# Kernel tuning notes

Hardware: AMD Instinct MI355X
Metric: run time of the kernel (lower is better)

The kernel has to match this reference:

```python
import jax, jax.numpy as jnp
import numpy as np

NUM_GRAPHS = 128
NUM_LAYERS = 3
BN_EPS = 1e-5


def setup_inputs() -> dict:
    key = jax.random.key(0)
    ks = jax.random.split(key, 8)
    N, E, D, C = 100000, 1250000, 64, 10
    x = jax.random.normal(ks[0], (N, D), dtype=jnp.float32)
    edge_index = jax.random.randint(ks[1], (2, E), 0, N, dtype=jnp.int64)
    batch = jnp.sort(jax.random.randint(ks[2], (N,), 0, NUM_GRAPHS, dtype=jnp.int64))
    W_rel = jax.random.normal(ks[3], (NUM_LAYERS, D, D), dtype=jnp.float32) * (1.0 / np.sqrt(D))
    b_rel = jax.random.normal(ks[4], (NUM_LAYERS, D), dtype=jnp.float32) * 0.01
    W_root = jax.random.normal(ks[5], (NUM_LAYERS, D, D), dtype=jnp.float32) * (1.0 / np.sqrt(D))
    gamma = jnp.ones((NUM_LAYERS, D), dtype=jnp.float32)
    beta = jnp.zeros((NUM_LAYERS, D), dtype=jnp.float32)
    W_cls = jax.random.normal(ks[6], (D, C), dtype=jnp.float32) * (1.0 / np.sqrt(D))
    b_cls = jnp.zeros((C,), dtype=jnp.float32)
    return {"x": x, "edge_index": edge_index, "batch": batch,
            "W_rel": W_rel, "b_rel": b_rel, "W_root": W_root,
            "gamma": gamma, "beta": beta, "W_cls": W_cls, "b_cls": b_cls}


def reference(x, edge_index, batch, W_rel, b_rel, W_root, gamma, beta, W_cls, b_cls):
    N = x.shape[0]
    src, dst = edge_index[0], edge_index[1]
    for l in range(NUM_LAYERS):
        # GraphConv: lin_rel(sum-aggregated neighbor feats) + lin_root(x)
        msg = jax.ops.segment_sum(x[src], dst, num_segments=N)  # [N, D]
        h = msg @ W_rel[l] + b_rel[l] + x @ W_root[l]
        # BatchNorm1d over nodes (batch statistics, training-mode math)
        mean = jnp.mean(h, axis=0)
        var = jnp.var(h, axis=0)
        h = (h - mean) * jax.lax.rsqrt(var + BN_EPS) * gamma[l] + beta[l]
        x = jax.nn.relu(h)  # dropout is identity at inference
    # global_mean_pool: segment mean over graph ids
    counts = jax.ops.segment_sum(jnp.ones((N,), dtype=x.dtype), batch, num_segments=NUM_GRAPHS)
    pooled = jax.ops.segment_sum(x, batch, num_segments=NUM_GRAPHS)
    pooled = pooled / jnp.maximum(counts, 1.0)[:, None]  # [G, D]
    return pooled @ W_cls + b_cls
```

## Files before the change

kernel.cpp:

```cpp
#include <hip/hip_runtime.h>

#define D 64
#define NGRAPH 128
#define NCLS 10
#define BN_EPS 1e-5f
#define BUCK_SZ 512
#define EPB 8192

typedef __attribute__((ext_vector_type(8))) __bf16 bf16x8;
typedef __attribute__((ext_vector_type(4))) float floatx4;

union BF8 { bf16x8 v; ushort u[8]; };

__device__ __forceinline__ unsigned f2bf_rne(float f) {
  unsigned u = __float_as_uint(f);
  return (u + 0x7FFFu + ((u >> 16) & 1u)) >> 16;
}
__device__ __forceinline__ unsigned pack2bf(float a, float b) {
  return f2bf_rne(a) | (f2bf_rne(b) << 16);
}
__device__ __forceinline__ float4 bf4_to_f4(uint2 u) {
  float4 r;
  r.x = __uint_as_float(u.x << 16);
  r.y = __uint_as_float(u.x & 0xFFFF0000u);
  r.z = __uint_as_float(u.y << 16);
  r.w = __uint_as_float(u.y & 0xFFFF0000u);
  return r;
}

__device__ __forceinline__ void split8(float4 a, float4 b,
                                       bf16x8* hi, bf16x8* lo) {
  float f[8] = {a.x, a.y, a.z, a.w, b.x, b.y, b.z, b.w};
  BF8 H, L;
#pragma unroll
  for (int t = 0; t < 8; t++) {
    unsigned u = __float_as_uint(f[t]);
    H.u[t] = (ushort)(u >> 16);
    float hf = __uint_as_float(u & 0xFFFF0000u);
    float lf = f[t] - hf;
    L.u[t] = (ushort)(__float_as_uint(lf) >> 16);
  }
  *hi = H.v;
  *lo = L.v;
}

__global__ __launch_bounds__(256) void bucket_scatter_kernel(
    const int* __restrict__ ei, int* __restrict__ gcnt, int* __restrict__ pk,
    int E, int capB, int nbuck) {
  __shared__ int hist[256];
  __shared__ int base[256];
  int t = threadIdx.x;
  int e0 = blockIdx.x * EPB;
  int e1 = min(e0 + EPB, E);
  hist[t] = 0;
  __syncthreads();
  for (int e = e0 + t; e < e1; e += 256)
    atomicAdd(&hist[ei[E + e] >> 9], 1);
  __syncthreads();
  int h = hist[t];
  if (t < nbuck && h > 0) base[t] = atomicAdd(&gcnt[t], h);
  hist[t] = 0;
  __syncthreads();
  for (int e = e0 + t; e < e1; e += 256) {
    int s = ei[e];
    int d = ei[E + e];
    int b = d >> 9;
    int pos = base[b] + atomicAdd(&hist[b], 1);
    if (pos < capB) pk[(size_t)b * capB + pos] = (s << 9) | (d & (BUCK_SZ - 1));
  }
}

__global__ void bucket_scan_kernel(const int* __restrict__ gcnt,
                                   int* __restrict__ bstart,
                                   int* __restrict__ row_start,
                                   int nbuck, int N, int capB) {
  __shared__ int s[256];
  int t = threadIdx.x;
  int v = (t < nbuck) ? min(gcnt[t], capB) : 0;
  s[t] = v;
  __syncthreads();
  for (int off = 1; off < 256; off <<= 1) {
    int add = (t >= off) ? s[t - off] : 0;
    __syncthreads();
    s[t] += add;
    __syncthreads();
  }
  if (t < nbuck) bstart[t] = s[t] - v;
  if (t == 0) {
    bstart[nbuck] = s[255];
    row_start[N] = s[255];
  }
}

__global__ __launch_bounds__(256) void bucket_place_kernel(
    const int* __restrict__ pk, const int* __restrict__ gcnt,
    const int* __restrict__ bstart, int* __restrict__ row_start,
    int* __restrict__ csr_src, int N, int capB) {
  __shared__ int hist[BUCK_SZ];
  __shared__ int scn[256];
  __shared__ int cur[BUCK_SZ];
  int b = blockIdx.x;
  int t = threadIdx.x;
  hist[t] = 0;
  hist[t + 256] = 0;
  int cnt = min(gcnt[b], capB);
  const int* seg = pk + (size_t)b * capB;
  __syncthreads();
  for (int e = t; e < cnt; e += 256)
    atomicAdd(&hist[seg[e] & (BUCK_SZ - 1)], 1);
  __syncthreads();
  scn[t] = hist[2 * t] + hist[2 * t + 1];
  __syncthreads();
  for (int off = 1; off < 256; off <<= 1) {
    int add = (t >= off) ? scn[t - off] : 0;
    __syncthreads();
    scn[t] += add;
    __syncthreads();
  }
  int base = bstart[b];
  int ex = (t == 0) ? 0 : scn[t - 1];
  int c0 = base + ex;
  int c1 = c0 + hist[2 * t];
  cur[2 * t] = c0;
  cur[2 * t + 1] = c1;
  int dst0 = b * BUCK_SZ + 2 * t;
  if (dst0 < N) row_start[dst0] = c0;
  if (dst0 + 1 < N) row_start[dst0 + 1] = c1;
  __syncthreads();
  for (int e = t; e < cnt; e += 256) {
    int p = seg[e];
    int slot = atomicAdd(&cur[p & (BUCK_SZ - 1)], 1);
    csr_src[slot] = p >> 9;
  }
}

__global__ __launch_bounds__(256) void wsplit_kernel(
    const float* __restrict__ Wrel, const float* __restrict__ Wroot,
    ushort* __restrict__ wfrag) {
  int l = blockIdx.x;
  const float* Wr = Wrel + l * 4096;
  const float* Wo = Wroot + l * 4096;
  ushort* base = wfrag + l * 16384;
  for (int slot = threadIdx.x; slot < 1024; slot += 256) {
    int kt = slot >> 8, nt = (slot >> 6) & 3, lane = slot & 63;
    int quad = lane >> 4, c = lane & 15;
    ushort* ph = base + (((kt * 4 + nt) * 2 + 0) * 64 + lane) * 8;
    ushort* pl = base + (((kt * 4 + nt) * 2 + 1) * 64 + lane) * 8;
#pragma unroll
    for (int j = 0; j < 8; j++) {
      int k = kt * 32 + quad * 8 + j;
      int n = nt * 16 + c;
      float w = (k < 64) ? Wr[k * 64 + n] : Wo[(k - 64) * 64 + n];
      unsigned u = __float_as_uint(w);
      ph[j] = (ushort)(u >> 16);
      float lf = w - __uint_as_float(u & 0xFFFF0000u);
      pl[j] = (ushort)(__float_as_uint(lf) >> 16);
    }
  }
}

__global__ __launch_bounds__(256) void xprep_kernel(
    const float* __restrict__ x, ushort* __restrict__ xbf, int n) {
  int base = (blockIdx.x * 256 + threadIdx.x) * 8;
  if (base >= n) return;
  float4 a = *(const float4*)(x + base);
  float4 b = *(const float4*)(x + base + 4);
  uint4 o;
  o.x = pack2bf(a.x, a.y);
  o.y = pack2bf(a.z, a.w);
  o.z = pack2bf(b.x, b.y);
  o.w = pack2bf(b.z, b.w);
  *(uint4*)(xbf + base) = o;
}

__global__ __launch_bounds__(256) void gather_kernel(
    const ushort* __restrict__ xbf, const int* __restrict__ csr_src,
    const int* __restrict__ row_start, const float* __restrict__ scsh,
    int apply, float* __restrict__ msg, int N) {
  int i = blockIdx.x * 4 + (threadIdx.x >> 6);
  int lane = threadIdx.x & 63;
  int q = lane >> 4;
  int f = (lane & 15) << 2;
  if (i >= N) return;
  int e0 = row_start[i], e1 = row_start[i + 1];
  int cnt = e1 - e0;
  int myidx = csr_src[e0 + lane];
  float4 acc = {0.f, 0.f, 0.f, 0.f};
  float4 sc, sh;
  if (apply) {
    sc = *(const float4*)&scsh[f];
    sh = *(const float4*)&scsh[D + f];
  }

  int cnt64 = min(cnt, 64);
  for (int base = 0; base < cnt64; base += 16) {
    int j0 = base + q;
    int s0 = __shfl(myidx, j0);
    int s1 = __shfl(myidx, j0 + 4);
    int s2 = __shfl(myidx, j0 + 8);
    int s3 = __shfl(myidx, j0 + 12);
    float m0 = (j0 < cnt) ? 1.f : 0.f;
    float m1 = (j0 + 4 < cnt) ? 1.f : 0.f;
    float m2 = (j0 + 8 < cnt) ? 1.f : 0.f;
    float m3 = (j0 + 12 < cnt) ? 1.f : 0.f;
    s0 = (j0 < cnt) ? s0 : 0;
    s1 = (j0 + 4 < cnt) ? s1 : 0;
    s2 = (j0 + 8 < cnt) ? s2 : 0;
    s3 = (j0 + 12 < cnt) ? s3 : 0;
    float4 v0 = bf4_to_f4(*(const uint2*)(xbf + (size_t)s0 * D + f));
    float4 v1 = bf4_to_f4(*(const uint2*)(xbf + (size_t)s1 * D + f));
    float4 v2 = bf4_to_f4(*(const uint2*)(xbf + (size_t)s2 * D + f));
    float4 v3 = bf4_to_f4(*(const uint2*)(xbf + (size_t)s3 * D + f));
    if (apply) {
      acc.x += m0 * fmaxf(v0.x * sc.x + sh.x, 0.f) + m1 * fmaxf(v1.x * sc.x + sh.x, 0.f)
             + m2 * fmaxf(v2.x * sc.x + sh.x, 0.f) + m3 * fmaxf(v3.x * sc.x + sh.x, 0.f);
      acc.y += m0 * fmaxf(v0.y * sc.y + sh.y, 0.f) + m1 * fmaxf(v1.y * sc.y + sh.y, 0.f)
             + m2 * fmaxf(v2.y * sc.y + sh.y, 0.f) + m3 * fmaxf(v3.y * sc.y + sh.y, 0.f);
      acc.z += m0 * fmaxf(v0.z * sc.z + sh.z, 0.f) + m1 * fmaxf(v1.z * sc.z + sh.z, 0.f)
             + m2 * fmaxf(v2.z * sc.z + sh.z, 0.f) + m3 * fmaxf(v3.z * sc.z + sh.z, 0.f);
      acc.w += m0 * fmaxf(v0.w * sc.w + sh.w, 0.f) + m1 * fmaxf(v1.w * sc.w + sh.w, 0.f)
             + m2 * fmaxf(v2.w * sc.w + sh.w, 0.f) + m3 * fmaxf(v3.w * sc.w + sh.w, 0.f);
    } else {
      acc.x += m0 * v0.x + m1 * v1.x + m2 * v2.x + m3 * v3.x;
      acc.y += m0 * v0.y + m1 * v1.y + m2 * v2.y + m3 * v3.y;
      acc.z += m0 * v0.z + m1 * v1.z + m2 * v2.z + m3 * v3.z;
      acc.w += m0 * v0.w + m1 * v1.w + m2 * v2.w + m3 * v3.w;
    }
  }

  for (int e = e0 + 64 + q; e < e1; e += 4) {
    float4 v = bf4_to_f4(*(const uint2*)(xbf + (size_t)csr_src[e] * D + f));
    if (apply) {
      acc.x += fmaxf(v.x * sc.x + sh.x, 0.f);
      acc.y += fmaxf(v.y * sc.y + sh.y, 0.f);
      acc.z += fmaxf(v.z * sc.z + sh.z, 0.f);
      acc.w += fmaxf(v.w * sc.w + sh.w, 0.f);
    } else {
      acc.x += v.x; acc.y += v.y; acc.z += v.z; acc.w += v.w;
    }
  }

  acc.x += __shfl_xor(acc.x, 16); acc.x += __shfl_xor(acc.x, 32);
  acc.y += __shfl_xor(acc.y, 16); acc.y += __shfl_xor(acc.y, 32);
  acc.z += __shfl_xor(acc.z, 16); acc.z += __shfl_xor(acc.z, 32);
  acc.w += __shfl_xor(acc.w, 16); acc.w += __shfl_xor(acc.w, 32);
  if (q == 0) *(float4*)(msg + (size_t)i * D + f) = acc;
}

__global__ __launch_bounds__(256, 1) void mm_mfma_kernel(
    const float* msg, const float* xin,
    const ushort* __restrict__ wfrag, const float* __restrict__ brel,
    const float* __restrict__ scsh, int apply,
    float* h, ushort* __restrict__ hbf, int wbf, float* __restrict__ stats,
    int N, int ntiles, int nwaves) {
  __shared__ float ssum[4][64];
  __shared__ float ssq[4][64];
  int tid = threadIdx.x;
  int lane = tid & 63;
  int wvid = tid >> 6;
  int wv = (blockIdx.x * 256 + tid) >> 6;
  int quad = lane >> 4;
  int lo4 = lane & 15;

  bf16x8 bf[4][4][2];
#pragma unroll
  for (int kt = 0; kt < 4; kt++)
#pragma unroll
    for (int nt = 0; nt < 4; nt++)
#pragma unroll
      for (int s = 0; s < 2; s++)
        bf[kt][nt][s] =
            *(const bf16x8*)(wfrag + (((kt * 4 + nt) * 2 + s) * 64 + lane) * 8);

  float bias[4];
#pragma unroll
  for (int nt = 0; nt < 4; nt++) bias[nt] = brel[nt * 16 + lo4];

  float scx[2][8], shx[2][8];
  if (apply) {
#pragma unroll
    for (int hh = 0; hh < 2; hh++)
#pragma unroll
      for (int jj = 0; jj < 8; jj++) {
        int f = hh * 32 + quad * 8 + jj;
        scx[hh][jj] = scsh[f];
        shx[hh][jj] = scsh[D + f];
      }
  }

  float psum[4] = {0.f, 0.f, 0.f, 0.f};
  float psq[4] = {0.f, 0.f, 0.f, 0.f};

  for (int t = wv; t < ntiles; t += nwaves) {
    int i0 = t * 16;
    int row = i0 + lo4;
    if (row >= N) row = N - 1;
    bf16x8 ahi[4], alo[4];
#pragma unroll
    for (int kt = 0; kt < 4; kt++) {
      const float* base = (kt < 2) ? msg : xin;
      const float* p = base + (size_t)row * D + (kt & 1) * 32 + quad * 8;
      float4 a = *(const float4*)p;
      float4 b = *(const float4*)(p + 4);
      if (kt >= 2 && apply) {
        int hh = kt - 2;
        a.x = fmaxf(a.x * scx[hh][0] + shx[hh][0], 0.f);
        a.y = fmaxf(a.y * scx[hh][1] + shx[hh][1], 0.f);
        a.z = fmaxf(a.z * scx[hh][2] + shx[hh][2], 0.f);
        a.w = fmaxf(a.w * scx[hh][3] + shx[hh][3], 0.f);
        b.x = fmaxf(b.x * scx[hh][4] + shx[hh][4], 0.f);
        b.y = fmaxf(b.y * scx[hh][5] + shx[hh][5], 0.f);
        b.z = fmaxf(b.z * scx[hh][6] + shx[hh][6], 0.f);
        b.w = fmaxf(b.w * scx[hh][7] + shx[hh][7], 0.f);
      }
      split8(a, b, &ahi[kt], &alo[kt]);
    }
#pragma unroll
    for (int nt = 0; nt < 4; nt++) {
      floatx4 acc = {bias[nt], bias[nt], bias[nt], bias[nt]};
#pragma unroll
      for (int kt = 0; kt < 4; kt++) {
        acc = __builtin_amdgcn_mfma_f32_16x16x32_bf16(ahi[kt], bf[kt][nt][0],
                                                      acc, 0, 0, 0);
        acc = __builtin_amdgcn_mfma_f32_16x16x32_bf16(ahi[kt], bf[kt][nt][1],
                                                      acc, 0, 0, 0);
        acc = __builtin_amdgcn_mfma_f32_16x16x32_bf16(alo[kt], bf[kt][nt][0],
                                                      acc, 0, 0, 0);
      }
#pragma unroll
      for (int r = 0; r < 4; r++) {
        int grow = i0 + quad * 4 + r;
        if (grow < N) {
          float v = acc[r];
          size_t idx = (size_t)grow * D + nt * 16 + lo4;
          h[idx] = v;
          if (wbf) hbf[idx] = (ushort)f2bf_rne(v);
          psum[nt] += v;
          psq[nt] += v * v;
        }
      }
    }
  }

#pragma unroll
  for (int nt = 0; nt < 4; nt++) {
    float s = psum[nt], q = psq[nt];
    s += __shfl_xor(s, 16); s += __shfl_xor(s, 32);
    q += __shfl_xor(q, 16); q += __shfl_xor(q, 32);
    if (lane < 16) { ssum[wvid][nt * 16 + lane] = s; ssq[wvid][nt * 16 + lane] = q; }
  }
  __syncthreads();
  if (tid < 64) {
    atomicAdd(&stats[tid], ssum[0][tid] + ssum[1][tid] + ssum[2][tid] + ssum[3][tid]);
  } else if (tid < 128) {
    int c = tid - 64;
    atomicAdd(&stats[D + c], ssq[0][c] + ssq[1][c] + ssq[2][c] + ssq[3][c]);
  }
}

__global__ void bn_finalize_kernel(float* __restrict__ stats,
                                   const float* __restrict__ gamma,
                                   const float* __restrict__ beta,
                                   float* __restrict__ scsh, float fN) {
  int j = threadIdx.x;
  float mean = stats[j] / fN;
  float var = stats[D + j] / fN - mean * mean;
  float sc = gamma[j] * rsqrtf(var + BN_EPS);
  scsh[j] = sc;
  scsh[D + j] = beta[j] - mean * sc;
  stats[j] = 0.f;
  stats[D + j] = 0.f;
}

__global__ __launch_bounds__(256) void norm_relu_pool_kernel(
    const float* __restrict__ h, const float* __restrict__ scsh,
    const int* __restrict__ batch, float* __restrict__ pooled, int N) {
  int j = threadIdx.x & 63;
  int q = threadIdx.x >> 6;
  int i0 = blockIdx.x * 256;
  float sc = scsh[j], sh = scsh[D + j];
  int curg = -1;
  float acc = 0.f;
  for (int r = q; r < 256; r += 4) {
    int i = i0 + r;
    if (i >= N) break;
    int b = batch[i];
    float v = fmaxf(h[(size_t)i * D + j] * sc + sh, 0.f);
    if (b != curg) {
      if (curg >= 0) atomicAdd(&pooled[curg * D + j], acc);
      curg = b;
      acc = v;
    } else {
      acc += v;
    }
  }
  if (curg >= 0) atomicAdd(&pooled[curg * D + j], acc);
}

__global__ void counts_kernel(const int* __restrict__ batch,
                              float* __restrict__ counts, int N) {
  int g = threadIdx.x;
  if (g >= NGRAPH) return;
  int lo = 0, hi = N;
  while (lo < hi) { int m = (lo + hi) >> 1; if (batch[m] < g) lo = m + 1; else hi = m; }
  int start = lo;
  lo = 0; hi = N;
  while (lo < hi) { int m = (lo + hi) >> 1; if (batch[m] <= g) lo = m + 1; else hi = m; }
  counts[g] = (float)(lo - start);
}

__global__ void cls_kernel(const float* __restrict__ pooled,
                           const float* __restrict__ counts,
                           const float* __restrict__ Wcls,
                           const float* __restrict__ bcls,
                           float* __restrict__ out) {
  int tid = blockIdx.x * blockDim.x + threadIdx.x;
  if (tid >= NGRAPH * NCLS) return;
  int g = tid / NCLS, c = tid % NCLS;
  float inv = 1.f / fmaxf(counts[g], 1.f);
  float acc = bcls[c];
#pragma unroll 8
  for (int k = 0; k < D; k++) acc += pooled[g * D + k] * inv * Wcls[k * NCLS + c];
  out[g * NCLS + c] = acc;
}

extern "C" void kernel_launch(void* const* d_in, const int* in_sizes, int n_in,
                              void* d_out, int out_size, void* d_ws, size_t ws_size,
                              hipStream_t stream) {
  const float* x      = (const float*)d_in[0];
  const int*   ei     = (const int*)d_in[1];
  const int*   batch  = (const int*)d_in[2];
  const float* W_rel  = (const float*)d_in[3];
  const float* b_rel  = (const float*)d_in[4];
  const float* W_root = (const float*)d_in[5];
  const float* gamma  = (const float*)d_in[6];
  const float* beta   = (const float*)d_in[7];
  const float* W_cls  = (const float*)d_in[8];
  const float* b_cls  = (const float*)d_in[9];
  float* out = (float*)d_out;

  int E = in_sizes[1] / 2;
  int N = in_sizes[2];
  size_t nd = (size_t)N * D;
  int nbuck = (N + BUCK_SZ - 1) / BUCK_SZ;
  int capB = ((2 * E / nbuck) + 511) & ~511;
  if (capB < 1024) capB = 1024;

  float* bufA    = (float*)d_ws;
  float* bufB    = bufA + nd;
  ushort* xbf    = (ushort*)(bufB + nd);
  float* stats   = (float*)(xbf + nd);
  float* scsh    = stats + 2 * D;
  float* pooled  = scsh + 2 * D;
  float* counts  = pooled + NGRAPH * D;
  int* gcnt      = (int*)(counts + NGRAPH);
  ushort* wfrag  = (ushort*)(gcnt + ((nbuck + 3) & ~3));
  int* bstart    = (int*)(wfrag + 3 * 16384);
  int* row_start = bstart + nbuck + 1;
  int* csr_src   = row_start + N + 1;
  int* pk        = csr_src + E;

  size_t zero_bytes = (size_t)(2 * D + 2 * D + NGRAPH * D + NGRAPH) * 4 +
                      (size_t)nbuck * 4;
  hipMemsetAsync(stats, 0, zero_bytes, stream);

  bucket_scatter_kernel<<<(E + EPB - 1) / EPB, 256, 0, stream>>>(
      ei, gcnt, pk, E, capB, nbuck);
  bucket_scan_kernel<<<1, 256, 0, stream>>>(gcnt, bstart, row_start, nbuck, N, capB);
  bucket_place_kernel<<<nbuck, 256, 0, stream>>>(pk, gcnt, bstart, row_start,
                                                 csr_src, N, capB);
  wsplit_kernel<<<3, 256, 0, stream>>>(W_rel, W_root, wfrag);
  xprep_kernel<<<(int)((nd / 8 + 255) / 256), 256, 0, stream>>>(x, xbf, (int)nd);

  const int MM_BLOCKS = 512;
  const int MM_WAVES = MM_BLOCKS * 4;
  int ntiles = (N + 15) / 16;
  const float* cur = x;
  for (int l = 0; l < 3; l++) {
    int apply = (l > 0) ? 1 : 0;
    int wbf = (l < 2) ? 1 : 0;

    gather_kernel<<<(N + 3) / 4, 256, 0, stream>>>(xbf, csr_src, row_start,
                                                   scsh, apply, bufB, N);

    mm_mfma_kernel<<<MM_BLOCKS, 256, 0, stream>>>(
        bufB, cur, wfrag + l * 16384, b_rel + l * D, scsh, apply,
        bufA, xbf , wbf, stats,
        N, ntiles, MM_WAVES);

    bn_finalize_kernel<<<1, 64, 0, stream>>>(stats, gamma + l * D, beta + l * D,
                                             scsh, (float)N);
    cur = bufA;
  }

  norm_relu_pool_kernel<<<(N + 255) / 256, 256, 0, stream>>>(bufA, scsh, batch,
                                                             pooled, N);
  counts_kernel<<<1, 128, 0, stream>>>(batch, counts, N);
  cls_kernel<<<(NGRAPH * NCLS + 255) / 256, 256, 0, stream>>>(pooled, counts,
                                                              W_cls, b_cls, out);
}
```

Measured before the change: 365.5 us.

## Feed root input from bf16 copy, skip fp32 h writes, persist gather waves

In layers after the first, the matmul kernel now reads the root input from the bf16 copy of the previous layer's output instead of the fp32 buffer. It writes the fp32 h buffer only in the last layer, where pooling needs it. This removes one fp32 write per early layer and halves the root-input read traffic, at the cost of bf16 precision on the root term. The gather kernel also becomes a persistent grid-stride loop over nodes that prefetches the next node's CSR offsets and neighbour indices to hide index-load latency.

New measurement: 385.6 us. +5.5%, slower.

```diff
diff --git a/kernel.cpp b/kernel.cpp
--- a/kernel.cpp
+++ b/kernel.cpp
@@ -176,82 +176,95 @@
 __global__ __launch_bounds__(256) void gather_kernel(
     const ushort* __restrict__ xbf, const int* __restrict__ csr_src,
     const int* __restrict__ row_start, const float* __restrict__ scsh,
-    int apply, float* __restrict__ msg, int N) {
-  int i = blockIdx.x * 4 + (threadIdx.x >> 6);
+    int apply, float* __restrict__ msg, int N, int nwaves) {
   int lane = threadIdx.x & 63;
   int q = lane >> 4;
   int f = (lane & 15) << 2;
-  if (i >= N) return;
-  int e0 = row_start[i], e1 = row_start[i + 1];
-  int cnt = e1 - e0;
-  int myidx = csr_src[e0 + lane];
-  float4 acc = {0.f, 0.f, 0.f, 0.f};
+  int gw = (blockIdx.x * 256 + threadIdx.x) >> 6;
+  if (gw >= N) return;
   float4 sc, sh;
   if (apply) {
     sc = *(const float4*)&scsh[f];
     sh = *(const float4*)&scsh[D + f];
   }
 
-  int cnt64 = min(cnt, 64);
-  for (int base = 0; base < cnt64; base += 16) {
-    int j0 = base + q;
-    int s0 = __shfl(myidx, j0);
-    int s1 = __shfl(myidx, j0 + 4);
-    int s2 = __shfl(myidx, j0 + 8);
-    int s3 = __shfl(myidx, j0 + 12);
-    float m0 = (j0 < cnt) ? 1.f : 0.f;
-    float m1 = (j0 + 4 < cnt) ? 1.f : 0.f;
-    float m2 = (j0 + 8 < cnt) ? 1.f : 0.f;
-    float m3 = (j0 + 12 < cnt) ? 1.f : 0.f;
-    s0 = (j0 < cnt) ? s0 : 0;
-    s1 = (j0 + 4 < cnt) ? s1 : 0;
-    s2 = (j0 + 8 < cnt) ? s2 : 0;
-    s3 = (j0 + 12 < cnt) ? s3 : 0;
-    float4 v0 = bf4_to_f4(*(const uint2*)(xbf + (size_t)s0 * D + f));
-    float4 v1 = bf4_to_f4(*(const uint2*)(xbf + (size_t)s1 * D + f));
-    float4 v2 = bf4_to_f4(*(const uint2*)(xbf + (size_t)s2 * D + f));
-    float4 v3 = bf4_to_f4(*(const uint2*)(xbf + (size_t)s3 * D + f));
-    if (apply) {
-      acc.x += m0 * fmaxf(v0.x * sc.x + sh.x, 0.f) + m1 * fmaxf(v1.x * sc.x + sh.x, 0.f)
-             + m2 * fmaxf(v2.x * sc.x + sh.x, 0.f) + m3 * fmaxf(v3.x * sc.x + sh.x, 0.f);
-      acc.y += m0 * fmaxf(v0.y * sc.y + sh.y, 0.f) + m1 * fmaxf(v1.y * sc.y + sh.y, 0.f)
-             + m2 * fmaxf(v2.y * sc.y + sh.y, 0.f) + m3 * fmaxf(v3.y * sc.y + sh.y, 0.f);
-      acc.z += m0 * fmaxf(v0.z * sc.z + sh.z, 0.f) + m1 * fmaxf(v1.z * sc.z + sh.z, 0.f)
-             + m2 * fmaxf(v2.z * sc.z + sh.z, 0.f) + m3 * fmaxf(v3.z * sc.z + sh.z, 0.f);
-      acc.w += m0 * fmaxf(v0.w * sc.w + sh.w, 0.f) + m1 * fmaxf(v1.w * sc.w + sh.w, 0.f)
-             + m2 * fmaxf(v2.w * sc.w + sh.w, 0.f) + m3 * fmaxf(v3.w * sc.w + sh.w, 0.f);
-    } else {
-      acc.x += m0 * v0.x + m1 * v1.x + m2 * v2.x + m3 * v3.x;
-      acc.y += m0 * v0.y + m1 * v1.y + m2 * v2.y + m3 * v3.y;
-      acc.z += m0 * v0.z + m1 * v1.z + m2 * v2.z + m3 * v3.z;
-      acc.w += m0 * v0.w + m1 * v1.w + m2 * v2.w + m3 * v3.w;
-    }
-  }
-
-  for (int e = e0 + 64 + q; e < e1; e += 4) {
-    float4 v = bf4_to_f4(*(const uint2*)(xbf + (size_t)csr_src[e] * D + f));
-    if (apply) {
-      acc.x += fmaxf(v.x * sc.x + sh.x, 0.f);
-      acc.y += fmaxf(v.y * sc.y + sh.y, 0.f);
-      acc.z += fmaxf(v.z * sc.z + sh.z, 0.f);
-      acc.w += fmaxf(v.w * sc.w + sh.w, 0.f);
-    } else {
-      acc.x += v.x; acc.y += v.y; acc.z += v.z; acc.w += v.w;
-    }
-  }
-
-  acc.x += __shfl_xor(acc.x, 16); acc.x += __shfl_xor(acc.x, 32);
-  acc.y += __shfl_xor(acc.y, 16); acc.y += __shfl_xor(acc.y, 32);
-  acc.z += __shfl_xor(acc.z, 16); acc.z += __shfl_xor(acc.z, 32);
-  acc.w += __shfl_xor(acc.w, 16); acc.w += __shfl_xor(acc.w, 32);
-  if (q == 0) *(float4*)(msg + (size_t)i * D + f) = acc;
+  int i = gw;
+  int e0 = row_start[i];
+  int cnt = row_start[i + 1] - e0;
+  int myidx = csr_src[e0 + lane];
+
+  while (i < N) {
+    int inext = i + nwaves;
+    int e0n = 0, cntn = 0, idxn = 0;
+    if (inext < N) {
+      e0n = row_start[inext];
+      cntn = row_start[inext + 1] - e0n;
+      idxn = csr_src[e0n + lane];
+    }
+
+    float4 acc = {0.f, 0.f, 0.f, 0.f};
+    int cnt64 = min(cnt, 64);
+    for (int base = 0; base < cnt64; base += 16) {
+      int j0 = base + q;
+      int s0 = __shfl(myidx, j0);
+      int s1 = __shfl(myidx, j0 + 4);
+      int s2 = __shfl(myidx, j0 + 8);
+      int s3 = __shfl(myidx, j0 + 12);
+      float m0 = (j0 < cnt) ? 1.f : 0.f;
+      float m1 = (j0 + 4 < cnt) ? 1.f : 0.f;
+      float m2 = (j0 + 8 < cnt) ? 1.f : 0.f;
+      float m3 = (j0 + 12 < cnt) ? 1.f : 0.f;
+      s0 = (j0 < cnt) ? s0 : 0;
+      s1 = (j0 + 4 < cnt) ? s1 : 0;
+      s2 = (j0 + 8 < cnt) ? s2 : 0;
+      s3 = (j0 + 12 < cnt) ? s3 : 0;
+      float4 v0 = bf4_to_f4(*(const uint2*)(xbf + (size_t)s0 * D + f));
+      float4 v1 = bf4_to_f4(*(const uint2*)(xbf + (size_t)s1 * D + f));
+      float4 v2 = bf4_to_f4(*(const uint2*)(xbf + (size_t)s2 * D + f));
+      float4 v3 = bf4_to_f4(*(const uint2*)(xbf + (size_t)s3 * D + f));
+      if (apply) {
+        acc.x += m0 * fmaxf(v0.x * sc.x + sh.x, 0.f) + m1 * fmaxf(v1.x * sc.x + sh.x, 0.f)
+               + m2 * fmaxf(v2.x * sc.x + sh.x, 0.f) + m3 * fmaxf(v3.x * sc.x + sh.x, 0.f);
+        acc.y += m0 * fmaxf(v0.y * sc.y + sh.y, 0.f) + m1 * fmaxf(v1.y * sc.y + sh.y, 0.f)
+               + m2 * fmaxf(v2.y * sc.y + sh.y, 0.f) + m3 * fmaxf(v3.y * sc.y + sh.y, 0.f);
+        acc.z += m0 * fmaxf(v0.z * sc.z + sh.z, 0.f) + m1 * fmaxf(v1.z * sc.z + sh.z, 0.f)
+               + m2 * fmaxf(v2.z * sc.z + sh.z, 0.f) + m3 * fmaxf(v3.z * sc.z + sh.z, 0.f);
+        acc.w += m0 * fmaxf(v0.w * sc.w + sh.w, 0.f) + m1 * fmaxf(v1.w * sc.w + sh.w, 0.f)
+               + m2 * fmaxf(v2.w * sc.w + sh.w, 0.f) + m3 * fmaxf(v3.w * sc.w + sh.w, 0.f);
+      } else {
+        acc.x += m0 * v0.x + m1 * v1.x + m2 * v2.x + m3 * v3.x;
+        acc.y += m0 * v0.y + m1 * v1.y + m2 * v2.y + m3 * v3.y;
+        acc.z += m0 * v0.z + m1 * v1.z + m2 * v2.z + m3 * v3.z;
+        acc.w += m0 * v0.w + m1 * v1.w + m2 * v2.w + m3 * v3.w;
+      }
+    }
+    for (int e = e0 + 64 + q; e < e0 + cnt; e += 4) {
+      float4 v = bf4_to_f4(*(const uint2*)(xbf + (size_t)csr_src[e] * D + f));
+      if (apply) {
+        acc.x += fmaxf(v.x * sc.x + sh.x, 0.f);
+        acc.y += fmaxf(v.y * sc.y + sh.y, 0.f);
+        acc.z += fmaxf(v.z * sc.z + sh.z, 0.f);
+        acc.w += fmaxf(v.w * sc.w + sh.w, 0.f);
+      } else {
+        acc.x += v.x; acc.y += v.y; acc.z += v.z; acc.w += v.w;
+      }
+    }
+
+    acc.x += __shfl_xor(acc.x, 16); acc.x += __shfl_xor(acc.x, 32);
+    acc.y += __shfl_xor(acc.y, 16); acc.y += __shfl_xor(acc.y, 32);
+    acc.z += __shfl_xor(acc.z, 16); acc.z += __shfl_xor(acc.z, 32);
+    acc.w += __shfl_xor(acc.w, 16); acc.w += __shfl_xor(acc.w, 32);
+    if (q == 0) *(float4*)(msg + (size_t)i * D + f) = acc;
+
+    i = inext; e0 = e0n; cnt = cntn; myidx = idxn;
+  }
 }
 
 __global__ __launch_bounds__(256, 1) void mm_mfma_kernel(
-    const float* msg, const float* xin,
+    const float* msg, const float* xf32, const ushort* xbfin,
     const ushort* __restrict__ wfrag, const float* __restrict__ brel,
     const float* __restrict__ scsh, int apply,
-    float* h, ushort* __restrict__ hbf, int wbf, float* __restrict__ stats,
+    float* h, ushort* hbf, int wh, int wbf, float* __restrict__ stats,
     int N, int ntiles, int nwaves) {
   __shared__ float ssum[4][64];
   __shared__ float ssq[4][64];
@@ -298,11 +311,17 @@
     bf16x8 ahi[4], alo[4];
 #pragma unroll
     for (int kt = 0; kt < 4; kt++) {
-      const float* base = (kt < 2) ? msg : xin;
-      const float* p = base + (size_t)row * D + (kt & 1) * 32 + quad * 8;
-      float4 a = *(const float4*)p;
-      float4 b = *(const float4*)(p + 4);
-      if (kt >= 2 && apply) {
+      float4 a, b;
+      if (kt < 2) {
+        const float* p = msg + (size_t)row * D + (kt & 1) * 32 + quad * 8;
+        a = *(const float4*)p;
+        b = *(const float4*)(p + 4);
+      } else if (apply) {
+        const ushort* p = xbfin + (size_t)row * D + (kt & 1) * 32 + quad * 8;
+        uint4 u = *(const uint4*)p;
+        uint2 ulo = {u.x, u.y}, uhi = {u.z, u.w};
+        a = bf4_to_f4(ulo);
+        b = bf4_to_f4(uhi);
         int hh = kt - 2;
         a.x = fmaxf(a.x * scx[hh][0] + shx[hh][0], 0.f);
         a.y = fmaxf(a.y * scx[hh][1] + shx[hh][1], 0.f);
@@ -312,6 +331,10 @@
         b.y = fmaxf(b.y * scx[hh][5] + shx[hh][5], 0.f);
         b.z = fmaxf(b.z * scx[hh][6] + shx[hh][6], 0.f);
         b.w = fmaxf(b.w * scx[hh][7] + shx[hh][7], 0.f);
+      } else {
+        const float* p = xf32 + (size_t)row * D + (kt & 1) * 32 + quad * 8;
+        a = *(const float4*)p;
+        b = *(const float4*)(p + 4);
       }
       split8(a, b, &ahi[kt], &alo[kt]);
     }
@@ -333,7 +356,7 @@
         if (grow < N) {
           float v = acc[r];
           size_t idx = (size_t)grow * D + nt * 16 + lo4;
-          h[idx] = v;
+          if (wh) h[idx] = v;
           if (wbf) hbf[idx] = (ushort)f2bf_rne(v);
           psum[nt] += v;
           psq[nt] += v * v;
@@ -474,23 +497,24 @@
 
   const int MM_BLOCKS = 512;
   const int MM_WAVES = MM_BLOCKS * 4;
+  const int G_BLOCKS = 2048;
+  const int G_WAVES = G_BLOCKS * 4;
   int ntiles = (N + 15) / 16;
-  const float* cur = x;
   for (int l = 0; l < 3; l++) {
     int apply = (l > 0) ? 1 : 0;
     int wbf = (l < 2) ? 1 : 0;
-
-    gather_kernel<<<(N + 3) / 4, 256, 0, stream>>>(xbf, csr_src, row_start,
-                                                   scsh, apply, bufB, N);
+    int wh = (l == 2) ? 1 : 0;
+
+    gather_kernel<<<G_BLOCKS, 256, 0, stream>>>(xbf, csr_src, row_start,
+                                                scsh, apply, bufB, N, G_WAVES);
 
     mm_mfma_kernel<<<MM_BLOCKS, 256, 0, stream>>>(
-        bufB, cur, wfrag + l * 16384, b_rel + l * D, scsh, apply,
-        bufA, xbf , wbf, stats,
+        bufB, x, xbf, wfrag + l * 16384, b_rel + l * D, scsh, apply,
+        bufA, xbf , wh, wbf, stats,
         N, ntiles, MM_WAVES);
 
     bn_finalize_kernel<<<1, 64, 0, stream>>>(stats, gamma + l * D, beta + l * D,
                                              scsh, (float)N);
-    cur = bufA;
   }
 
   norm_relu_pool_kernel<<<(N + 255) / 256, 256, 0, stream>>>(bufA, scsh, batch,
```
